# Kernel tuning notes

Hardware: AMD Instinct MI355X
Metric: run time of the kernel (lower is better)

Reference implementation:

```python
import jax, jax.numpy as jnp
import numpy as np

NTOKENS = 8192
H = 1024
FFN = 2048
NEXPERTS = 64
TOPK = 2
M = NTOKENS * TOPK  # total routed slots


def setup_inputs() -> dict:
    key = jax.random.key(0)
    k1, k2, k3 = jax.random.split(key, 3)
    inputs_shard = jax.random.normal(k1, (NTOKENS, H), dtype=jnp.float32)
    w1 = jax.random.normal(k2, (NEXPERTS, H, FFN), dtype=jnp.float32) * 0.02
    w2 = jax.random.normal(k3, (NEXPERTS, FFN, H), dtype=jnp.float32) * 0.02
    # Balanced routing: each expert receives exactly M // NEXPERTS slots.
    rng = np.random.default_rng(0)
    per_expert = M // NEXPERTS
    eid_flat = rng.permutation(np.repeat(np.arange(M // per_expert), per_expert))  # [M] expert id per (token,k)
    order = np.argsort(eid_flat, kind='stable')  # slot -> flat (token,k) index
    scatter_flat = np.empty(M, dtype=np.int64)
    scatter_flat[order] = np.arange(M)  # (token,k) -> slot in expert-sorted buffer
    scatter_index = jnp.asarray(scatter_flat.reshape(NTOKENS, TOPK))
    splits = jnp.full((NEXPERTS,), per_expert, dtype=jnp.int64)
    return {"inputs_shard": inputs_shard, "w1": w1, "w2": w2,
            "scatter_index": scatter_index, "splits": splits}


def reference(inputs_shard, w1, w2, scatter_index, splits):
    ntokens, topk = scatter_index.shape
    m = ntokens * topk
    nexperts = w1.shape[0]
    per_expert = m // nexperts  # splits are balanced by construction
    # AG-scatter: place each token copy into its expert-sorted slot.
    slot_to_tk = jnp.argsort(scatter_index.reshape(-1))  # slot -> (token,k) flat idx
    token = slot_to_tk // topk                            # slot -> source token
    expanded = inputs_shard[token]                        # [M, H]
    # Grouped GEMM 1 (h -> ffn) + exact gelu, per expert block.
    xg = expanded.reshape(nexperts, per_expert, -1)       # [G, M/G, H]
    h1 = jnp.einsum('geh,ghf->gef', xg, w1)               # [G, M/G, FFN]
    a = jax.nn.gelu(h1, approximate=False)
    # Grouped GEMM 2 (ffn -> h).
    h2 = jnp.einsum('gef,gfh->geh', a, w2).reshape(m, -1)  # [M, H]
    # Gather-RS: gather topk partials per token and reduce (sum).
    out = h2[scatter_index.reshape(-1)].reshape(ntokens, topk, -1).sum(axis=1)
    return out
```

## Files before the change

### kernel.cpp

```cpp
#include <hip/hip_runtime.h>
#include <hip/hip_bf16.h>
#include <math.h>

#define NTOK 8192
#define HD   1024
#define FFND 2048
#define NE   64
#define MTOT 16384
#define PER_E 256

typedef __attribute__((ext_vector_type(8))) short bh8;
typedef __attribute__((ext_vector_type(4))) float f4;
typedef unsigned short u16;
typedef unsigned int   u32;

__device__ __forceinline__ u16 f2bf(float f) {
  union { float f; u32 u; } x; x.f = f;
  u32 r = x.u + 0x7fffu + ((x.u >> 16) & 1u);
  return (u16)(r >> 16);
}

__device__ __forceinline__ float bf2f(u16 b) {
  union { u32 u; float f; } x; x.u = ((u32)b) << 16; return x.f;
}

__device__ __forceinline__ u32 pk2(float lo, float hi) {
  __hip_bfloat162 h = __float22bfloat162_rn(make_float2(lo, hi));
  union { __hip_bfloat162 h; u32 u; } c; c.h = h;
  return c.u;
}

__global__ void k_build_s2t(const int* __restrict__ sidx, int* __restrict__ s2t) {
  int i = blockIdx.x * 256 + threadIdx.x;
  s2t[sidx[i]] = i >> 1;
}

__global__ void k_gather_x(const float* __restrict__ inp, const int* __restrict__ s2t,
                           u16* __restrict__ X) {
  int idx = blockIdx.x * 256 + threadIdx.x;
  int slot = idx >> 7;
  int c    = idx & 127;
  const float* src = inp + (size_t)s2t[slot] * HD + c * 8;
  float v[8];
  *(f4*)(v)     = *(const f4*)(src);
  *(f4*)(v + 4) = *(const f4*)(src + 4);
  u32 o[4];
  #pragma unroll
  for (int j = 0; j < 4; ++j) o[j] = pk2(v[2 * j], v[2 * j + 1]);
  *(uint4*)(X + (size_t)slot * HD + c * 8) = *(uint4*)o;
}

template<int K, int N, bool GELU>
__global__ __launch_bounds__(512, 2)
void moe_gemm(const u16* __restrict__ Abf, const float* __restrict__ Bf,
              u16* __restrict__ outp)
{
  constexpr int BM = 256, BN = 256, BK = 64;
  constexpr int NB = N / BN;
  constexpr int NT = K / BK;
  constexpr int NF = 8;
  constexpr int BITER = 4;
  constexpr int ABYTES = BM * 128;
  __shared__ __align__(16) char lds[2 * ABYTES + BN * 128];
  char* Bs = lds + 2 * ABYTES;

  const int d = blockIdx.y * NB + blockIdx.x;
  const int x = d & 7, j = d >> 3;
  const int e  = x * (NE / 8) + j / NB;
  const int n0 = (j % NB) * BN;
  const int row0 = e * PER_E;
  const int tid  = threadIdx.x;
  const int lane = tid & 63, wid = tid >> 6;
  const int wr   = wid >> 1, wc = wid & 1;

  const u16*   Arow = Abf + (size_t)row0 * K;
  const float* Bsrc = Bf + (size_t)e * K * N + n0;

  auto stageA = [&](int buf, int k0) {
    char* dst = lds + buf * ABYTES;
    #pragma unroll
    for (int i = 0; i < 4; ++i) {
      int c = i * 512 + tid;
      int r = c >> 3, kc = c & 7;
      int kswz = kc ^ (r & 7);
      __builtin_amdgcn_global_load_lds(
          (const void*)(Arow + (size_t)r * K + k0 + kswz * 8),
          (void*)(dst + c * 16), 16, 0, 0);
    }
  };
  auto loadB = [&](float* br, int k0) {
    #pragma unroll
    for (int i = 0; i < BITER; ++i) {
      int c = i * 512 + tid;
      int n = c & (BN - 1), kc = c / BN;
      const float* p = Bsrc + (size_t)(k0 + kc * 8) * N + n;
      #pragma unroll
      for (int jj = 0; jj < 8; ++jj) br[i * 8 + jj] = p[(size_t)jj * N];
    }
  };
  auto writeB = [&](const float* br) {
    #pragma unroll
    for (int i = 0; i < BITER; ++i) {
      int c = i * 512 + tid;
      int n = c & (BN - 1), kc = c / BN;
      u32 q[4];
      #pragma unroll
      for (int jj = 0; jj < 4; ++jj) q[jj] = pk2(br[i * 8 + 2 * jj], br[i * 8 + 2 * jj + 1]);
      *(uint4*)(Bs + n * 128 + ((kc * 16) ^ ((n & 7) << 4))) = *(uint4*)q;
    }
  };

  f4 acc[4][NF] = {};
  float breg[BITER * 8];

  loadB(breg, 0);
  __builtin_amdgcn_sched_barrier(0);
  stageA(0, 0);
  asm volatile("s_waitcnt vmcnt(4)" ::: "memory");
  __builtin_amdgcn_sched_barrier(0);
  writeB(breg);
  asm volatile("s_waitcnt lgkmcnt(0)" ::: "memory");
  __builtin_amdgcn_sched_barrier(0);
  __builtin_amdgcn_s_barrier();
  __builtin_amdgcn_sched_barrier(0);

  int cur = 0;
  for (int t = 0; t < NT; ++t) {
    const char* As = lds + cur * ABYTES;
    if (t + 1 < NT) {
      loadB(breg, (t + 1) * BK);
      __builtin_amdgcn_sched_barrier(0);
      stageA(cur ^ 1, (t + 1) * BK);
      asm volatile("s_waitcnt vmcnt(36)" ::: "memory");
    } else {
      asm volatile("s_waitcnt vmcnt(0)" ::: "memory");
    }
    __builtin_amdgcn_sched_barrier(0);
    __builtin_amdgcn_s_setprio(1);
    #pragma unroll
    for (int kk = 0; kk < 2; ++kk) {
      int kByte = kk * 64 + ((lane >> 4) << 4);
      bh8 a[4], b[NF];
      #pragma unroll
      for (int m = 0; m < 4; ++m) {
        int r = wr * 64 + m * 16 + (lane & 15);
        a[m] = *(const bh8*)(As + r * 128 + (kByte ^ ((r & 7) << 4)));
      }
      #pragma unroll
      for (int n = 0; n < NF; ++n) {
        int r = wc * 128 + n * 16 + (lane & 15);
        b[n] = *(const bh8*)(Bs + r * 128 + (kByte ^ ((r & 7) << 4)));
      }
      #pragma unroll
      for (int m = 0; m < 4; ++m)
        #pragma unroll
        for (int n = 0; n < NF; ++n)
          acc[m][n] = __builtin_amdgcn_mfma_f32_16x16x32_bf16(a[m], b[n], acc[m][n], 0, 0, 0);
    }
    __builtin_amdgcn_s_setprio(0);
    __builtin_amdgcn_s_barrier();
    __builtin_amdgcn_sched_barrier(0);
    if (t + 1 < NT) {
      asm volatile("s_waitcnt vmcnt(4)" ::: "memory");
      __builtin_amdgcn_sched_barrier(0);
      writeB(breg);
      asm volatile("s_waitcnt lgkmcnt(0)" ::: "memory");
      __builtin_amdgcn_sched_barrier(0);
      __builtin_amdgcn_s_barrier();
      __builtin_amdgcn_sched_barrier(0);
      cur ^= 1;
    }
  }

  #pragma unroll
  for (int m = 0; m < 4; ++m) {
    #pragma unroll
    for (int n = 0; n < NF; ++n) {
      int rowb = wr * 64 + m * 16 + ((lane >> 4) << 2);
      int col  = n0 + wc * 128 + n * 16 + (lane & 15);
      #pragma unroll
      for (int jj = 0; jj < 4; ++jj) {
        float xv = acc[m][n][jj];
        if (GELU) {
          float y = fminf(fmaxf(xv, -8.f), 8.f);
          float u = 0.7978845608f * (y + 0.044715f * y * y * y);
          float t2 = __expf(-2.f * u);
          float g = __fdividef(y, 1.f + t2);
          outp[(size_t)(row0 + rowb + jj) * N + col] = f2bf(g);
        } else {
          outp[(size_t)(row0 + rowb + jj) * N + col] = f2bf(xv);
        }
      }
    }
  }
}

__global__ void k_reduce(const u16* __restrict__ h2, const int* __restrict__ sidx,
                         float* __restrict__ out) {
  int t = blockIdx.x;
  int c = threadIdx.x;
  const u16* r0 = h2 + (size_t)sidx[2 * t] * HD + c * 4;
  const u16* r1 = h2 + (size_t)sidx[2 * t + 1] * HD + c * 4;
  u16 a0[4], a1[4];
  *(uint2*)a0 = *(const uint2*)r0;
  *(uint2*)a1 = *(const uint2*)r1;
  f4 s;
  #pragma unroll
  for (int jj = 0; jj < 4; ++jj) s[jj] = bf2f(a0[jj]) + bf2f(a1[jj]);
  *(f4*)(out + (size_t)t * HD + c * 4) = s;
}

extern "C" void kernel_launch(void* const* d_in, const int* in_sizes, int n_in,
                              void* d_out, int out_size, void* d_ws, size_t ws_size,
                              hipStream_t stream) {
  const float* inp  = (const float*)d_in[0];
  const float* w1   = (const float*)d_in[1];
  const float* w2   = (const float*)d_in[2];
  const int*   sidx = (const int*)d_in[3];
  float* out = (float*)d_out;

  char* ws   = (char*)d_ws;
  int*   s2t = (int*)ws;
  u16*   X   = (u16*)(ws + (1 << 20));
  u16*   act = (u16*)(ws + (1 << 20) + (32u << 20));
  u16*   h2  = (u16*)(ws + (1 << 20) + (96u << 20));

  k_build_s2t<<<MTOT / 256, 256, 0, stream>>>(sidx, s2t);
  k_gather_x<<<(MTOT * (HD / 8)) / 256, 256, 0, stream>>>(inp, s2t, X);
  moe_gemm<HD, FFND, true><<<dim3(FFND / 256, NE), 512, 0, stream>>>(X, w1, act);
  moe_gemm<FFND, HD, false><<<dim3(HD / 256, NE), 512, 0, stream>>>(act, w2, h2);
  k_reduce<<<NTOK, 256, 0, stream>>>(h2, sidx, out);
}
```

Baseline: 292.3 us.

## Fuse all MoE stages into one cooperative persistent kernel with grid syncs

Replaces the five separate launches (index build, gather, two grouped GEMMs, reduce) with a single cooperative kernel of 256 blocks that runs each stage in grid-stride loops separated by grid.sync(). The aim is to remove per-launch overhead and the gaps between kernels. In exchange, GEMM1 now runs its 512 tiles as two sequential waves per block. Grid-wide barriers add sync cost, and the gather and reduce stages run on fewer threads than before.

```diff
diff --git a/kernel.cpp b/kernel.cpp
--- a/kernel.cpp
+++ b/kernel.cpp
@@ -1,6 +1,9 @@
 #include <hip/hip_runtime.h>
+#include <hip/hip_cooperative_groups.h>
 #include <hip/hip_bf16.h>
 #include <math.h>
+
+namespace cg = cooperative_groups;
 
 #define NTOK 8192
 #define HD   1024
@@ -8,6 +11,8 @@
 #define NE   64
 #define MTOT 16384
 #define PER_E 256
+#define NBLK 256
+#define NTHR 512
 
 typedef __attribute__((ext_vector_type(8))) short bh8;
 typedef __attribute__((ext_vector_type(4))) float f4;
@@ -30,30 +35,10 @@
   return c.u;
 }
 
-__global__ void k_build_s2t(const int* __restrict__ sidx, int* __restrict__ s2t) {
-  int i = blockIdx.x * 256 + threadIdx.x;
-  s2t[sidx[i]] = i >> 1;
-}
-
-__global__ void k_gather_x(const float* __restrict__ inp, const int* __restrict__ s2t,
-                           u16* __restrict__ X) {
-  int idx = blockIdx.x * 256 + threadIdx.x;
-  int slot = idx >> 7;
-  int c    = idx & 127;
-  const float* src = inp + (size_t)s2t[slot] * HD + c * 8;
-  float v[8];
-  *(f4*)(v)     = *(const f4*)(src);
-  *(f4*)(v + 4) = *(const f4*)(src + 4);
-  u32 o[4];
-  #pragma unroll
-  for (int j = 0; j < 4; ++j) o[j] = pk2(v[2 * j], v[2 * j + 1]);
-  *(uint4*)(X + (size_t)slot * HD + c * 8) = *(uint4*)o;
-}
-
 template<int K, int N, bool GELU>
-__global__ __launch_bounds__(512, 2)
-void moe_gemm(const u16* __restrict__ Abf, const float* __restrict__ Bf,
-              u16* __restrict__ outp)
+__device__ __forceinline__ void gemm_tile(char* lds, const u16* __restrict__ Abf,
+                                          const float* __restrict__ Bf,
+                                          u16* __restrict__ outp, int d, int tid)
 {
   constexpr int BM = 256, BN = 256, BK = 64;
   constexpr int NB = N / BN;
@@ -61,15 +46,12 @@
   constexpr int NF = 8;
   constexpr int BITER = 4;
   constexpr int ABYTES = BM * 128;
-  __shared__ __align__(16) char lds[2 * ABYTES + BN * 128];
   char* Bs = lds + 2 * ABYTES;
 
-  const int d = blockIdx.y * NB + blockIdx.x;
   const int x = d & 7, j = d >> 3;
   const int e  = x * (NE / 8) + j / NB;
   const int n0 = (j % NB) * BN;
   const int row0 = e * PER_E;
-  const int tid  = threadIdx.x;
   const int lane = tid & 63, wid = tid >> 6;
   const int wr   = wid >> 1, wc = wid & 1;
 
@@ -195,19 +177,53 @@
   }
 }
 
-__global__ void k_reduce(const u16* __restrict__ h2, const int* __restrict__ sidx,
-                         float* __restrict__ out) {
-  int t = blockIdx.x;
-  int c = threadIdx.x;
-  const u16* r0 = h2 + (size_t)sidx[2 * t] * HD + c * 4;
-  const u16* r1 = h2 + (size_t)sidx[2 * t + 1] * HD + c * 4;
-  u16 a0[4], a1[4];
-  *(uint2*)a0 = *(const uint2*)r0;
-  *(uint2*)a1 = *(const uint2*)r1;
-  f4 s;
-  #pragma unroll
-  for (int jj = 0; jj < 4; ++jj) s[jj] = bf2f(a0[jj]) + bf2f(a1[jj]);
-  *(f4*)(out + (size_t)t * HD + c * 4) = s;
+__global__ __launch_bounds__(NTHR, 2)
+void moe_fused(const float* __restrict__ inp, const float* __restrict__ w1,
+               const float* __restrict__ w2, const int* __restrict__ sidx,
+               float* __restrict__ out, int* __restrict__ s2t,
+               u16* __restrict__ X, u16* __restrict__ act, u16* __restrict__ h2)
+{
+  constexpr int ABYTES = 256 * 128;
+  __shared__ __align__(16) char lds[2 * ABYTES + 256 * 128];
+  cg::grid_group grid = cg::this_grid();
+  const int tid = threadIdx.x, bid = blockIdx.x;
+  const int gt = bid * NTHR + tid, gstride = NBLK * NTHR;
+
+  for (int i = gt; i < MTOT; i += gstride) s2t[sidx[i]] = i >> 1;
+  grid.sync();
+
+  for (int idx = gt; idx < MTOT * (HD / 8); idx += gstride) {
+    int slot = idx >> 7, c = idx & 127;
+    const float* src = inp + (size_t)s2t[slot] * HD + c * 8;
+    float v[8];
+    *(f4*)(v)     = *(const f4*)(src);
+    *(f4*)(v + 4) = *(const f4*)(src + 4);
+    u32 o[4];
+    #pragma unroll
+    for (int j = 0; j < 4; ++j) o[j] = pk2(v[2 * j], v[2 * j + 1]);
+    *(uint4*)(X + (size_t)slot * HD + c * 8) = *(uint4*)o;
+  }
+  grid.sync();
+
+  for (int tl = bid; tl < NE * (FFND / 256); tl += NBLK)
+    gemm_tile<HD, FFND, true>(lds, X, w1, act, tl, tid);
+  grid.sync();
+
+  gemm_tile<FFND, HD, false>(lds, act, w2, h2, bid, tid);
+  grid.sync();
+
+  for (int i = gt; i < NTOK * (HD / 4); i += gstride) {
+    int t = i >> 8, c = i & 255;
+    const u16* r0 = h2 + (size_t)sidx[2 * t] * HD + c * 4;
+    const u16* r1 = h2 + (size_t)sidx[2 * t + 1] * HD + c * 4;
+    u16 a0[4], a1[4];
+    *(uint2*)a0 = *(const uint2*)r0;
+    *(uint2*)a1 = *(const uint2*)r1;
+    f4 s;
+    #pragma unroll
+    for (int jj = 0; jj < 4; ++jj) s[jj] = bf2f(a0[jj]) + bf2f(a1[jj]);
+    *(f4*)(out + (size_t)t * HD + c * 4) = s;
+  }
 }
 
 extern "C" void kernel_launch(void* const* d_in, const int* in_sizes, int n_in,
@@ -225,9 +241,8 @@
   u16*   act = (u16*)(ws + (1 << 20) + (32u << 20));
   u16*   h2  = (u16*)(ws + (1 << 20) + (96u << 20));
 
-  k_build_s2t<<<MTOT / 256, 256, 0, stream>>>(sidx, s2t);
-  k_gather_x<<<(MTOT * (HD / 8)) / 256, 256, 0, stream>>>(inp, s2t, X);
-  moe_gemm<HD, FFND, true><<<dim3(FFND / 256, NE), 512, 0, stream>>>(X, w1, act);
-  moe_gemm<FFND, HD, false><<<dim3(HD / 256, NE), 512, 0, stream>>>(act, w2, h2);
-  k_reduce<<<NTOK, 256, 0, stream>>>(h2, sidx, out);
-}
+  void* args[] = { (void*)&inp, (void*)&w1, (void*)&w2, (void*)&sidx,
+                   (void*)&out, (void*)&s2t, (void*)&X, (void*)&act, (void*)&h2 };
+  hipLaunchCooperativeKernel((const void*)moe_fused, dim3(NBLK), dim3(NTHR),
+                             args, 0, stream);
+}
```

Result: slower. 430.0 us (+47.1%).

## Double-buffer B tile in LDS and prefetch weights two k-steps ahead

Applied to the files above, without the earlier changes.

The weight (B) tile now has two LDS buffers, and two register staging sets alternate so the fp32 weights for step t+2 load while step t computes. The bf16 conversion and LDS write for step t+1 move ahead of the MFMA loop, which leaves one barrier per k-iteration instead of two. This aims to hide the global-load latency of the fp32 weight stream and remove a synchronization point. In exchange it uses 32 KB more LDS and 32 more staging registers per thread, which could cost occupancy or cause spills under the 512x2 launch bound.

```diff
diff --git a/kernel.cpp b/kernel.cpp
--- a/kernel.cpp
+++ b/kernel.cpp
@@ -13,6 +13,8 @@
 typedef __attribute__((ext_vector_type(4))) float f4;
 typedef unsigned short u16;
 typedef unsigned int   u32;
+
+#define SB0 __builtin_amdgcn_sched_barrier(0)
 
 __device__ __forceinline__ u16 f2bf(float f) {
   union { float f; u32 u; } x; x.f = f;
@@ -61,8 +63,8 @@
   constexpr int NF = 8;
   constexpr int BITER = 4;
   constexpr int ABYTES = BM * 128;
-  __shared__ __align__(16) char lds[2 * ABYTES + BN * 128];
-  char* Bs = lds + 2 * ABYTES;
+  constexpr int BBYTES = BN * 128;
+  __shared__ __align__(16) char lds[2 * ABYTES + 2 * BBYTES];
 
   const int d = blockIdx.y * NB + blockIdx.x;
   const int x = d & 7, j = d >> 3;
@@ -98,7 +100,8 @@
       for (int jj = 0; jj < 8; ++jj) br[i * 8 + jj] = p[(size_t)jj * N];
     }
   };
-  auto writeB = [&](const float* br) {
+  auto writeB = [&](int buf, const float* br) {
+    char* dst = lds + 2 * ABYTES + buf * BBYTES;
     #pragma unroll
     for (int i = 0; i < BITER; ++i) {
       int c = i * 512 + tid;
@@ -106,36 +109,35 @@
       u32 q[4];
       #pragma unroll
       for (int jj = 0; jj < 4; ++jj) q[jj] = pk2(br[i * 8 + 2 * jj], br[i * 8 + 2 * jj + 1]);
-      *(uint4*)(Bs + n * 128 + ((kc * 16) ^ ((n & 7) << 4))) = *(uint4*)q;
+      *(uint4*)(dst + n * 128 + ((kc * 16) ^ ((n & 7) << 4))) = *(uint4*)q;
     }
   };
 
   f4 acc[4][NF] = {};
-  float breg[BITER * 8];
-
-  loadB(breg, 0);
-  __builtin_amdgcn_sched_barrier(0);
-  stageA(0, 0);
-  asm volatile("s_waitcnt vmcnt(4)" ::: "memory");
-  __builtin_amdgcn_sched_barrier(0);
-  writeB(breg);
+  float breg0[BITER * 8], breg1[BITER * 8];
+
+  loadB(breg0, 0); SB0;
+  stageA(0, 0); SB0;
+  loadB(breg1, BK); SB0;
+  asm volatile("s_waitcnt vmcnt(36)" ::: "memory");
+  SB0;
+  writeB(0, breg0);
   asm volatile("s_waitcnt lgkmcnt(0)" ::: "memory");
-  __builtin_amdgcn_sched_barrier(0);
+  SB0;
   __builtin_amdgcn_s_barrier();
-  __builtin_amdgcn_sched_barrier(0);
-
-  int cur = 0;
+  SB0;
+
   for (int t = 0; t < NT; ++t) {
+    const int cur = t & 1;
     const char* As = lds + cur * ABYTES;
-    if (t + 1 < NT) {
-      loadB(breg, (t + 1) * BK);
-      __builtin_amdgcn_sched_barrier(0);
-      stageA(cur ^ 1, (t + 1) * BK);
-      asm volatile("s_waitcnt vmcnt(36)" ::: "memory");
-    } else {
-      asm volatile("s_waitcnt vmcnt(0)" ::: "memory");
-    }
-    __builtin_amdgcn_sched_barrier(0);
+    const char* Bs = lds + 2 * ABYTES + cur * BBYTES;
+    if (t + 2 < NT) { loadB((t & 1) ? breg1 : breg0, (t + 2) * BK); SB0; }
+    if (t + 1 < NT) { stageA(cur ^ 1, (t + 1) * BK); SB0; }
+    if (t + 2 < NT)      asm volatile("s_waitcnt vmcnt(36)" ::: "memory");
+    else if (t + 1 < NT) asm volatile("s_waitcnt vmcnt(4)"  ::: "memory");
+    else                 asm volatile("s_waitcnt vmcnt(0)"  ::: "memory");
+    SB0;
+    if (t + 1 < NT) writeB(cur ^ 1, ((t + 1) & 1) ? breg1 : breg0);
     __builtin_amdgcn_s_setprio(1);
     #pragma unroll
     for (int kk = 0; kk < 2; ++kk) {
@@ -158,18 +160,10 @@
           acc[m][n] = __builtin_amdgcn_mfma_f32_16x16x32_bf16(a[m], b[n], acc[m][n], 0, 0, 0);
     }
     __builtin_amdgcn_s_setprio(0);
+    asm volatile("s_waitcnt lgkmcnt(0)" ::: "memory");
+    SB0;
     __builtin_amdgcn_s_barrier();
-    __builtin_amdgcn_sched_barrier(0);
-    if (t + 1 < NT) {
-      asm volatile("s_waitcnt vmcnt(4)" ::: "memory");
-      __builtin_amdgcn_sched_barrier(0);
-      writeB(breg);
-      asm volatile("s_waitcnt lgkmcnt(0)" ::: "memory");
-      __builtin_amdgcn_sched_barrier(0);
-      __builtin_amdgcn_s_barrier();
-      __builtin_amdgcn_sched_barrier(0);
-      cur ^= 1;
-    }
+    SB0;
   }
 
   #pragma unroll
```

Result: slower. 930.1 us (+218.2%).
